# Kernel tuning notes

Hardware: AMD Instinct MI355X
Metric: run time of the kernel (lower is better)

Reference implementation:

```python
import jax, jax.numpy as jnp
import numpy as np

B, S, D, R, H, NI, NP, NO, K = 2, 2048, 1024, 1024, 8, 8, 32, 8, 3
DH = R // H


def setup_inputs() -> dict:
    key = jax.random.key(0)
    ks = jax.random.split(key, 32)
    rn = lambda k, shp, s=1.0: jax.random.normal(k, shp, jnp.float32) * s
    nrm = lambda v: v / (jnp.linalg.norm(v, axis=-1, keepdims=True) + 1e-8)
    w = 1.0 / np.sqrt(D).astype(np.float32)
    inp = {
        'x': rn(ks[0], (B, S, D)),
        'mask': jnp.tril(jnp.ones((S, S), bool))[None, None],  # causal [1,1,S,S]
        'Wr_in': rn(ks[1], (NI, D), w), 'Wr_proc': rn(ks[2], (NP, D), w), 'Wr_out': rn(ks[3], (NO, D), w),
        'WrO_in': rn(ks[4], (NI, R), w), 'WrO_proc': rn(ks[5], (NP, R), w), 'WrO_out': rn(ks[6], (NO, R), w),
        'Wq_in': rn(ks[7], (NI, D, R), w), 'vq': nrm(rn(ks[8], (NP, R))), 'Wq_out': rn(ks[9], (NO, R, D), w),
        'Wk_in': rn(ks[10], (NI, D, R), w), 'vk': nrm(rn(ks[11], (NP, R))), 'Wk_out': rn(ks[12], (NO, R, D), w),
        'Wv_in': rn(ks[13], (NI, D, R), w), 'vv': nrm(rn(ks[14], (NP, R))), 'Wv_out': rn(ks[15], (NO, R, D), w),
        # circuit_O = NeuronCircuit(rank, d_model): dims swapped
        'Wo_in': rn(ks[16], (NI, R, D), w), 'vo': nrm(rn(ks[17], (NP, D))), 'Wo_out': rn(ks[18], (NO, D, R), w),
    }
    return inp


def _router(x, Wi, Wp, Wo, k):
    in_w = jax.nn.softmax(x @ Wi.T, axis=-1)            # [B,S,NI]
    _, proc_idx = jax.lax.top_k(x @ Wp.T, k)            # [B,S,k]
    out_w = jax.nn.softmax(x @ Wo.T, axis=-1)           # [B,S,NO]
    return in_w, proc_idx, out_w


def _circuit(x, Win, vproc, Wout, in_w, proc_idx, out_w):
    # soft input mix: d_in -> r
    h = jnp.einsum('bsd,ndr,bsn->bsr', x, Win, in_w)
    # k sequential Householder reflections with gathered vectors
    v = vproc[proc_idx]                                 # [B,S,k,r]
    v = v / jnp.sqrt(jnp.sum(v * v, axis=-1, keepdims=True) + 1e-8)
    for i in range(v.shape[2]):
        vi = v[:, :, i, :]
        h = h - 2.0 * vi * jnp.sum(h * vi, axis=-1, keepdims=True)
    # soft output mix: r -> d_out
    return jnp.einsum('bsr,nrd,bsn->bsd', h, Wout, out_w)


def reference(x, mask, Wr_in, Wr_proc, Wr_out, WrO_in, WrO_proc, WrO_out,
              Wq_in, vq, Wq_out, Wk_in, vk, Wk_out, Wv_in, vv, Wv_out,
              Wo_in, vo, Wo_out):
    in_w, pidx, out_w = _router(x, Wr_in, Wr_proc, Wr_out, K)
    Q = _circuit(x, Wq_in, vq, Wq_out, in_w, pidx, out_w)   # [B,S,R]
    Kt = _circuit(x, Wk_in, vk, Wk_out, in_w, pidx, out_w)
    V = _circuit(x, Wv_in, vv, Wv_out, in_w, pidx, out_w)
    q = Q.reshape(B, S, H, DH).transpose(0, 2, 1, 3)
    k = Kt.reshape(B, S, H, DH).transpose(0, 2, 1, 3)
    v = V.reshape(B, S, H, DH).transpose(0, 2, 1, 3)
    scores = jnp.einsum('bhqd,bhkd->bhqk', q, k) / np.sqrt(DH).astype(np.float32)
    scores = jnp.where(mask, scores, jnp.float32(-1e9))
    p = jax.nn.softmax(scores, axis=-1)
    o = jnp.einsum('bhqk,bhkd->bhqd', p, v)
    o = o.transpose(0, 2, 1, 3).reshape(B, S, R)
    in_wO, pidxO, out_wO = _router(o, WrO_in, WrO_proc, WrO_out, K)
    out = _circuit(o, Wo_in, vo, Wo_out, in_wO, pidxO, out_wO)  # [B,S,D]
    return out
```

## Files before the change

### kernel.cpp

```cpp
#include <hip/hip_runtime.h>


typedef __attribute__((ext_vector_type(4))) float f32x4;
typedef _Float16 f16x8 __attribute__((ext_vector_type(8)));
typedef _Float16 f16x4 __attribute__((ext_vector_type(4)));

static constexpr int S_LEN  = 2048;
static constexpr int TOK    = 4096;
static constexpr int DMODEL = 1024;
static constexpr int KDIM   = 8192;

__device__ __forceinline__ void async16(const void* g, void* l) {
  __builtin_amdgcn_global_load_lds(
      (const __attribute__((address_space(1))) void*)g,
      (__attribute__((address_space(3))) void*)l, 16, 0, 0);
}

__global__ __launch_bounds__(256) void transpose_split(const float* __restrict__ W,
                                                       _Float16* __restrict__ Th,
                                                       _Float16* __restrict__ Tl) {
  __shared__ float tbuf[64][65];
  const int tid = threadIdx.x;
  const int k0 = blockIdx.x * 64, n0 = blockIdx.y * 64;
#pragma unroll
  for (int j = 0; j < 4; ++j) {
    int ci = tid + 256 * j;
    int r = ci >> 4, c4 = (ci & 15) * 4;
    float4 v = *(const float4*)&W[(size_t)(k0 + r) * DMODEL + n0 + c4];
    tbuf[r][c4 + 0] = v.x; tbuf[r][c4 + 1] = v.y;
    tbuf[r][c4 + 2] = v.z; tbuf[r][c4 + 3] = v.w;
  }
  __syncthreads();
#pragma unroll
  for (int j = 0; j < 2; ++j) {
    int ci = tid + 256 * j;
    int nl = ci >> 3, k8 = (ci & 7) * 8;
    f16x8 hv, lv;
#pragma unroll
    for (int e = 0; e < 8; ++e) {
      float v = tbuf[k8 + e][nl];
      _Float16 hh = (_Float16)v;
      hv[e] = hh;
      lv[e] = (_Float16)(v - (float)hh);
    }
    size_t off = (size_t)(n0 + nl) * KDIM + k0 + k8;
    *(f16x8*)&Th[off] = hv;
    if (Tl != nullptr) *(f16x8*)&Tl[off] = lv;
  }
}

__global__ __launch_bounds__(256) void router_kernel(const float* __restrict__ X,
                                                     const float* __restrict__ Wi,
                                                     const float* __restrict__ Wp,
                                                     const float* __restrict__ Wo,
                                                     float* __restrict__ in_w,
                                                     float* __restrict__ out_w,
                                                     int* __restrict__ pidx,
                                                     _Float16* __restrict__ Xh,
                                                     _Float16* __restrict__ Xl) {
  __shared__ float xs[1024];
  __shared__ double lg[48];
  const int t = blockIdx.x, tid = threadIdx.x;
  const int wid = tid >> 6, lane = tid & 63;
#pragma unroll
  for (int j = 0; j < 4; ++j) {
    int d = tid + 256 * j;
    xs[d] = X[(size_t)t * DMODEL + d];
  }
  __syncthreads();
  for (int i = wid; i < 48; i += 4) {
    const float* wrow = (i < 8)  ? Wi + (size_t)i * DMODEL
                      : (i < 40) ? Wp + (size_t)(i - 8) * DMODEL
                                 : Wo + (size_t)(i - 40) * DMODEL;
    double s = 0.0;
#pragma unroll
    for (int j = 0; j < 16; ++j) { int d = lane + 64 * j; s += (double)xs[d] * (double)wrow[d]; }
#pragma unroll
    for (int mm = 32; mm >= 1; mm >>= 1) s += __shfl_xor(s, mm);
    if (lane == 0) lg[i] = s;
  }
  __syncthreads();
  if (tid == 0) {
    float l[8], m;
    for (int i = 0; i < 8; ++i) l[i] = (float)lg[i];
    m = l[0];
    for (int i = 1; i < 8; ++i) m = fmaxf(m, l[i]);
    float e[8], su = 0.f;
    for (int i = 0; i < 8; ++i) { e[i] = expf(l[i] - m); su += e[i]; }
    for (int i = 0; i < 8; ++i) in_w[t * 8 + i] = e[i] / su;
  } else if (tid == 64) {
    float l[8], m;
    for (int i = 0; i < 8; ++i) l[i] = (float)lg[40 + i];
    m = l[0];
    for (int i = 1; i < 8; ++i) m = fmaxf(m, l[i]);
    float e[8], su = 0.f;
    for (int i = 0; i < 8; ++i) { e[i] = expf(l[i] - m); su += e[i]; }
    for (int i = 0; i < 8; ++i) out_w[t * 8 + i] = e[i] / su;
  } else if (tid == 128) {
    unsigned used = 0;
    for (int j = 0; j < 3; ++j) {
      double best = -1e300; int bi = 0;
      for (int i = 0; i < 32; ++i)
        if (!((used >> i) & 1u) && lg[8 + i] > best) { best = lg[8 + i]; bi = i; }
      used |= 1u << bi;
      pidx[t * 3 + j] = bi;
    }
  }
  if (Xh != nullptr) {
#pragma unroll
    for (int j = 0; j < 4; ++j) {
      int d = tid + 256 * j;
      float v = xs[d];
      _Float16 hh = (_Float16)v;
      Xh[(size_t)t * DMODEL + d] = hh;
      Xl[(size_t)t * DMODEL + d] = (_Float16)(v - (float)hh);
    }
  }
}

__global__ __launch_bounds__(256) void reflect4_kernel(const float* __restrict__ Pa,
                                                       const float* __restrict__ Pb,
                                                       const float* __restrict__ Pc,
                                                       const float* __restrict__ Pd,
                                                       const int* __restrict__ pidx,
                                                       const float* __restrict__ vtab,
                                                       _Float16* __restrict__ Hh,
                                                       _Float16* __restrict__ Hl) {
  __shared__ float red[8];
  const int t = blockIdx.x, tid = threadIdx.x;
  const int wid = tid >> 6, lane = tid & 63;
  size_t gi = (size_t)t * DMODEL + tid * 4;
  float4 ha = *(const float4*)&Pa[gi];
  float4 hb = *(const float4*)&Pb[gi];
  float4 hc = *(const float4*)&Pc[gi];
  float4 hd = *(const float4*)&Pd[gi];
  float4 h = {ha.x + hb.x + hc.x + hd.x, ha.y + hb.y + hc.y + hd.y,
              ha.z + hb.z + hc.z + hd.z, ha.w + hb.w + hc.w + hd.w};
  for (int i = 0; i < 3; ++i) {
    int idx = pidx[t * 3 + i];
    float4 vi = *(const float4*)&vtab[(size_t)idx * DMODEL + tid * 4];
    float hv = h.x * vi.x + h.y * vi.y + h.z * vi.z + h.w * vi.w;
    float vv = vi.x * vi.x + vi.y * vi.y + vi.z * vi.z + vi.w * vi.w;
#pragma unroll
    for (int mm = 32; mm >= 1; mm >>= 1) { hv += __shfl_xor(hv, mm); vv += __shfl_xor(vv, mm); }
    if (lane == 0) { red[wid] = hv; red[4 + wid] = vv; }
    __syncthreads();
    float dot = red[0] + red[1] + red[2] + red[3];
    float vn  = red[4] + red[5] + red[6] + red[7];
    __syncthreads();
    float c = 2.f * dot / (vn + 1e-8f);
    h.x -= c * vi.x; h.y -= c * vi.y; h.z -= c * vi.z; h.w -= c * vi.w;
  }
  float a[4] = {h.x, h.y, h.z, h.w};
  f16x4 hv4, lv4;
#pragma unroll
  for (int e = 0; e < 4; ++e) {
    _Float16 hh = (_Float16)a[e];
    hv4[e] = hh;
    lv4[e] = (_Float16)(a[e] - (float)hh);
  }
  *(f16x4*)&Hh[gi] = hv4;
  *(f16x4*)&Hl[gi] = lv4;
}

__global__ __launch_bounds__(256) void reduce4_planes(const float* __restrict__ a,
                                                      const float* __restrict__ b,
                                                      const float* __restrict__ c,
                                                      const float* __restrict__ d,
                                                      _Float16* __restrict__ Dh,
                                                      _Float16* __restrict__ Dl) {
  size_t i = ((size_t)blockIdx.x * 256 + threadIdx.x) * 4;
  float4 va = *(const float4*)&a[i];
  float4 vb = *(const float4*)&b[i];
  float4 vc = *(const float4*)&c[i];
  float4 vd = *(const float4*)&d[i];
  float s[4] = {va.x + vb.x + vc.x + vd.x, va.y + vb.y + vc.y + vd.y,
                va.z + vb.z + vc.z + vd.z, va.w + vb.w + vc.w + vd.w};
  f16x4 hv, lv;
#pragma unroll
  for (int e = 0; e < 4; ++e) {
    _Float16 hh = (_Float16)s[e];
    hv[e] = hh;
    lv[e] = (_Float16)(s[e] - (float)hh);
  }
  *(f16x4*)&Dh[i] = hv;
  *(f16x4*)&Dl[i] = lv;
}

__global__ __launch_bounds__(256) void reduce4_f32(const float* __restrict__ a,
                                                   const float* __restrict__ b,
                                                   const float* __restrict__ c,
                                                   const float* __restrict__ d,
                                                   float* __restrict__ o) {
  size_t i = ((size_t)blockIdx.x * 256 + threadIdx.x) * 4;
  float4 va = *(const float4*)&a[i];
  float4 vb = *(const float4*)&b[i];
  float4 vc = *(const float4*)&c[i];
  float4 vd = *(const float4*)&d[i];
  float4 vo = {va.x + vb.x + vc.x + vd.x, va.y + vb.y + vc.y + vd.y,
               va.z + vb.z + vc.z + vd.z, va.w + vb.w + vc.w + vd.w};
  *(float4*)&o[i] = vo;
}

template <bool FAST>
__global__ __launch_bounds__(512, 2) void gemm_planes(const _Float16* __restrict__ Ahp,
                                                      const _Float16* __restrict__ Alp,
                                                      const float* __restrict__ wmix,
                                                      const _Float16* __restrict__ Bh,
                                                      const _Float16* __restrict__ Bl,
                                                      float* __restrict__ C0,
                                                      float* __restrict__ C1,
                                                      float* __restrict__ C2,
                                                      float* __restrict__ C3) {
  __shared__ _Float16 sAh[2][256 * 32];
  __shared__ _Float16 sBh[2][256 * 32];
  __shared__ _Float16 sAl[2][FAST ? 8 : 256 * 32];
  __shared__ _Float16 sBl[2][FAST ? 8 : 256 * 32];
  __shared__ float sWr[256 * 2];
  const int tid = threadIdx.x;
  const int wid = tid >> 6, lane = tid & 63;
  const int l16 = lane & 15, lhi = lane >> 4;
  const int wr = wid >> 2, wc = wid & 3;
  const int fid = blockIdx.x + (blockIdx.y << 4) + (blockIdx.z << 6);
  const int wg  = ((fid & 7) << 5) + (fid >> 3);
  const int bm = (wg & 15) * 256;
  const int bn = ((wg >> 4) & 3) * 256;
  const int kz = wg >> 6;
  const int kbase = kz * 2048, nb = kz * 2;
  float* __restrict__ Cp = (kz == 0) ? C0 : (kz == 1) ? C1 : (kz == 2) ? C2 : C3;

  {
    int row = tid >> 1, p = tid & 1;
    const float* w = &wmix[(size_t)(bm + row) * 8 + nb];
    sWr[tid] = p ? w[1] : w[0] / w[1];
  }

  f32x4 acc[8][4];
#pragma unroll
  for (int i = 0; i < 8; ++i)
#pragma unroll
    for (int j = 0; j < 4; ++j) { f32x4 z = {0.f, 0.f, 0.f, 0.f}; acc[i][j] = z; }

  auto STAGE = [&](int buf, int kt) {
    const int kg = kbase + kt, d0 = kg & 1023;
#pragma unroll
    for (int j = 0; j < 2; ++j) {
      int ci = tid + 512 * j;
      int row = ci >> 2, jc = ci & 3;
      int jcs = jc ^ ((row >> 1) & 3);
      size_t ga = (size_t)(bm + row) * DMODEL + d0 + jcs * 8;
      size_t gb = (size_t)(bn + row) * KDIM + kg + jcs * 8;
      async16(&Ahp[ga], &sAh[buf][ci * 8]);
      async16(&Bh[gb],  &sBh[buf][ci * 8]);
      if constexpr (!FAST) {
        async16(&Alp[ga], &sAl[buf][ci * 8]);
        async16(&Bl[gb],  &sBl[buf][ci * 8]);
      }
    }
  };

  auto COMPUTE = [&](int buf) {
    __builtin_amdgcn_s_setprio(1);
    f16x8 b_h[4], b_l[4];
#pragma unroll
    for (int ni = 0; ni < 4; ++ni) {
      int row = wc * 64 + ni * 16 + l16;
      int idx = row * 32 + ((lhi ^ ((row >> 1) & 3)) * 8);
      b_h[ni] = *(const f16x8*)&sBh[buf][idx];
      if constexpr (!FAST) b_l[ni] = *(const f16x8*)&sBl[buf][idx];
    }
#pragma unroll
    for (int mi = 0; mi < 8; ++mi) {
      int rowa = wr * 128 + mi * 16 + l16;
      int idxa = rowa * 32 + ((lhi ^ ((rowa >> 1) & 3)) * 8);
      f16x8 a_h = *(const f16x8*)&sAh[buf][idxa];
      f16x8 a_l;
      if constexpr (!FAST) a_l = *(const f16x8*)&sAl[buf][idxa];
#pragma unroll
      for (int ni = 0; ni < 4; ++ni) {
        f32x4 a = acc[mi][ni];
        a = __builtin_amdgcn_mfma_f32_16x16x32_f16(a_h, b_h[ni], a, 0, 0, 0);
        if constexpr (!FAST) {
          a = __builtin_amdgcn_mfma_f32_16x16x32_f16(a_h, b_l[ni], a, 0, 0, 0);
          a = __builtin_amdgcn_mfma_f32_16x16x32_f16(a_l, b_h[ni], a, 0, 0, 0);
        }
        acc[mi][ni] = a;
      }
    }
    __builtin_amdgcn_s_setprio(0);
  };

  STAGE(0, 0);
  for (int t = 0; t < 63; ++t) {
    STAGE((t + 1) & 1, (t + 1) * 32);
    if constexpr (FAST) asm volatile("s_waitcnt vmcnt(4)" ::: "memory");
    else                asm volatile("s_waitcnt vmcnt(8)" ::: "memory");
    __builtin_amdgcn_s_barrier();
    __builtin_amdgcn_sched_barrier(0);
    COMPUTE(t & 1);
    if (t == 31) {
#pragma unroll
      for (int mi = 0; mi < 8; ++mi)
#pragma unroll
        for (int r = 0; r < 4; ++r) {
          float s = sWr[(wr * 128 + mi * 16 + lhi * 4 + r) * 2];
#pragma unroll
          for (int ni = 0; ni < 4; ++ni) acc[mi][ni][r] *= s;
        }
    }
    __builtin_amdgcn_s_barrier();
  }
  asm volatile("s_waitcnt vmcnt(0)" ::: "memory");
  __builtin_amdgcn_s_barrier();
  __builtin_amdgcn_sched_barrier(0);
  COMPUTE(1);

#pragma unroll
  for (int mi = 0; mi < 8; ++mi)
#pragma unroll
    for (int r = 0; r < 4; ++r) {
      int rowl = wr * 128 + mi * 16 + lhi * 4 + r;
      float s = sWr[rowl * 2 + 1];
#pragma unroll
      for (int ni = 0; ni < 4; ++ni) {
        int col = bn + wc * 64 + ni * 16 + l16;
        Cp[(size_t)(bm + rowl) * DMODEL + col] = acc[mi][ni][r] * s;
      }
    }
}

__global__ __launch_bounds__(256) void vtrans4_kernel(const float* __restrict__ Va,
                                                      const float* __restrict__ Vb,
                                                      const float* __restrict__ Vc,
                                                      const float* __restrict__ Vd,
                                                      _Float16* __restrict__ Vth,
                                                      _Float16* __restrict__ Vtl) {
  __shared__ float tbuf[64][65];
  const int tid = threadIdx.x;
  const int t0 = blockIdx.x * 64, d0 = blockIdx.y * 64, bh = blockIdx.z;
  const int b = bh >> 3, h = bh & 7;
#pragma unroll
  for (int j = 0; j < 4; ++j) {
    int ci = tid + 256 * j;
    int r = ci >> 4, c4 = (ci & 15) * 4;
    size_t g = (size_t)(b * S_LEN + t0 + r) * DMODEL + h * 128 + d0 + c4;
    float4 va = *(const float4*)&Va[g];
    float4 vb = *(const float4*)&Vb[g];
    float4 vc = *(const float4*)&Vc[g];
    float4 vd = *(const float4*)&Vd[g];
    tbuf[r][c4 + 0] = va.x + vb.x + vc.x + vd.x;
    tbuf[r][c4 + 1] = va.y + vb.y + vc.y + vd.y;
    tbuf[r][c4 + 2] = va.z + vb.z + vc.z + vd.z;
    tbuf[r][c4 + 3] = va.w + vb.w + vc.w + vd.w;
  }
  __syncthreads();
#pragma unroll
  for (int j = 0; j < 4; ++j) {
    int ci = tid + 256 * j;
    int r = ci >> 4, c4 = (ci & 15) * 4;
    float s[4] = {tbuf[c4 + 0][r], tbuf[c4 + 1][r], tbuf[c4 + 2][r], tbuf[c4 + 3][r]};
    f16x4 hv, lv;
#pragma unroll
    for (int e = 0; e < 4; ++e) {
      _Float16 hh = (_Float16)s[e];
      hv[e] = hh;
      lv[e] = (_Float16)(s[e] - (float)hh);
    }
    size_t o = ((size_t)bh * 128 + d0 + r) * S_LEN + t0 + c4;
    *(f16x4*)&Vth[o] = hv;
    *(f16x4*)&Vtl[o] = lv;
  }
}

__global__ __launch_bounds__(256) void attn_kernel(const _Float16* __restrict__ Qh,
                                                   const _Float16* __restrict__ Ql,
                                                   const _Float16* __restrict__ Kh,
                                                   const _Float16* __restrict__ Kl,
                                                   const _Float16* __restrict__ Vth,
                                                   const _Float16* __restrict__ Vtl,
                                                   float* __restrict__ O,
                                                   _Float16* __restrict__ Oh) {
  __shared__ _Float16 sKh[32 * 128], sKl[32 * 128];
  __shared__ _Float16 sVh[128 * 32], sVl[128 * 32];
  __shared__ _Float16 sPh[4 * 16 * 32], sPl[4 * 16 * 32];
  const int tid = threadIdx.x;
  const int wid = tid >> 6, lane = tid & 63;
  const int l16 = lane & 15, lhi = lane >> 4;
  const int qt = (gridDim.x - 1) - blockIdx.x;
  const int bh = blockIdx.y;
  const int b = bh >> 3, h = bh & 7;
  const size_t qkbase = (size_t)b * S_LEN * DMODEL + h * 128;
  const float scale = 0.08838834764831845f;

  const int qrow = qt * 64 + wid * 16 + l16;
  const size_t qoff = qkbase + (size_t)qrow * DMODEL;
  f16x8 qh[4], ql[4];
#pragma unroll
  for (int kk = 0; kk < 4; ++kk) {
    qh[kk] = *(const f16x8*)&Qh[qoff + kk * 32 + lhi * 8];
    ql[kk] = *(const f16x8*)&Ql[qoff + kk * 32 + lhi * 8];
  }

  f32x4 of[8];
#pragma unroll
  for (int i = 0; i < 8; ++i) { f32x4 z = {0.f, 0.f, 0.f, 0.f}; of[i] = z; }
  float m_[4], l_[4];
#pragma unroll
  for (int r = 0; r < 4; ++r) { m_[r] = -1e30f; l_[r] = 0.f; }

  const int ntw = qt * 2 + 1 + (wid >> 1);
  const int NT  = qt * 2 + 2;

  for (int kt = 0; kt < NT; ++kt) {
    __syncthreads();
#pragma unroll
    for (int j = 0; j < 2; ++j) {
      int ci = tid + 256 * j;
      int k = ci >> 4, c = ci & 15;
      int cs = c ^ (k & 7);
      size_t g = qkbase + (size_t)(kt * 32 + k) * DMODEL + cs * 8;
      async16(&Kh[g], &sKh[k * 128 + c * 8]);
      async16(&Kl[g], &sKl[k * 128 + c * 8]);
    }
#pragma unroll
    for (int j = 0; j < 2; ++j) {
      int ci = tid + 256 * j;
      int d = ci >> 2, c = ci & 3;
      int cs = c ^ ((d >> 1) & 3);
      size_t g = ((size_t)bh * 128 + d) * S_LEN + kt * 32 + cs * 8;
      async16(&Vth[g], &sVh[d * 32 + c * 8]);
      async16(&Vtl[g], &sVl[d * 32 + c * 8]);
    }
    __syncthreads();

    if (kt < ntw) {
      f32x4 s0 = {0.f, 0.f, 0.f, 0.f}, s1 = {0.f, 0.f, 0.f, 0.f};
#pragma unroll
      for (int kk = 0; kk < 4; ++kk) {
        int col = (kk * 32 + lhi * 8);
        int i0 = l16 * 128 + (col ^ ((l16 & 7) * 8));
        int i1 = (16 + l16) * 128 + (col ^ (((16 + l16) & 7) * 8));
        f16x8 kb0h = *(const f16x8*)&sKh[i0];
        f16x8 kb0l = *(const f16x8*)&sKl[i0];
        f16x8 kb1h = *(const f16x8*)&sKh[i1];
        f16x8 kb1l = *(const f16x8*)&sKl[i1];
        s0 = __builtin_amdgcn_mfma_f32_16x16x32_f16(qh[kk], kb0h, s0, 0, 0, 0);
        s0 = __builtin_amdgcn_mfma_f32_16x16x32_f16(qh[kk], kb0l, s0, 0, 0, 0);
        s0 = __builtin_amdgcn_mfma_f32_16x16x32_f16(ql[kk], kb0h, s0, 0, 0, 0);
        s1 = __builtin_amdgcn_mfma_f32_16x16x32_f16(qh[kk], kb1h, s1, 0, 0, 0);
        s1 = __builtin_amdgcn_mfma_f32_16x16x32_f16(qh[kk], kb1l, s1, 0, 0, 0);
        s1 = __builtin_amdgcn_mfma_f32_16x16x32_f16(ql[kk], kb1h, s1, 0, 0, 0);
      }
      const int qg = qt * 64 + wid * 16 + (lane >> 4) * 4;
      if (kt == ntw - 1) {
#pragma unroll
        for (int r = 0; r < 4; ++r) {
          int q = qg + r;
          int k0 = kt * 32 + l16, k1 = k0 + 16;
          s0[r] = (k0 <= q) ? s0[r] * scale : -1e30f;
          s1[r] = (k1 <= q) ? s1[r] * scale : -1e30f;
        }
      } else {
#pragma unroll
        for (int r = 0; r < 4; ++r) { s0[r] *= scale; s1[r] *= scale; }
      }
      float p0[4], p1[4], fr[4];
#pragma unroll
      for (int r = 0; r < 4; ++r) {
        float rm = fmaxf(s0[r], s1[r]);
        rm = fmaxf(rm, __shfl_xor(rm, 1));
        rm = fmaxf(rm, __shfl_xor(rm, 2));
        rm = fmaxf(rm, __shfl_xor(rm, 4));
        rm = fmaxf(rm, __shfl_xor(rm, 8));
        float mn = fmaxf(m_[r], rm);
        fr[r] = __expf(m_[r] - mn);
        m_[r] = mn;
        p0[r] = __expf(s0[r] - mn);
        p1[r] = __expf(s1[r] - mn);
        float rs = p0[r] + p1[r];
        rs += __shfl_xor(rs, 1);
        rs += __shfl_xor(rs, 2);
        rs += __shfl_xor(rs, 4);
        rs += __shfl_xor(rs, 8);
        l_[r] = l_[r] * fr[r] + rs;
      }
#pragma unroll
      for (int i = 0; i < 8; ++i)
#pragma unroll
        for (int r = 0; r < 4; ++r) of[i][r] *= fr[r];
#pragma unroll
      for (int r = 0; r < 4; ++r) {
        int q = (lane >> 4) * 4 + r;
        int swz = ((q >> 1) & 3) * 8;
        int c0 = l16, c1 = 16 + l16;
        _Float16 h0 = (_Float16)p0[r];
        _Float16 h1 = (_Float16)p1[r];
        sPh[wid * 512 + q * 32 + (c0 ^ swz)] = h0;
        sPl[wid * 512 + q * 32 + (c0 ^ swz)] = (_Float16)(p0[r] - (float)h0);
        sPh[wid * 512 + q * 32 + (c1 ^ swz)] = h1;
        sPl[wid * 512 + q * 32 + (c1 ^ swz)] = (_Float16)(p1[r] - (float)h1);
      }
      int pidxr = wid * 512 + l16 * 32 + ((lhi * 8) ^ (((l16 >> 1) & 3) * 8));
      f16x8 pah = *(const f16x8*)&sPh[pidxr];
      f16x8 pal = *(const f16x8*)&sPl[pidxr];
#pragma unroll
      for (int d16 = 0; d16 < 8; ++d16) {
        int d = d16 * 16 + l16;
        int vidx = d * 32 + ((lhi * 8) ^ (((d >> 1) & 3) * 8));
        f16x8 vbh = *(const f16x8*)&sVh[vidx];
        f16x8 vbl = *(const f16x8*)&sVl[vidx];
        f32x4 a = of[d16];
        a = __builtin_amdgcn_mfma_f32_16x16x32_f16(pah, vbh, a, 0, 0, 0);
        a = __builtin_amdgcn_mfma_f32_16x16x32_f16(pah, vbl, a, 0, 0, 0);
        a = __builtin_amdgcn_mfma_f32_16x16x32_f16(pal, vbh, a, 0, 0, 0);
        of[d16] = a;
      }
    }
  }
  float inv[4];
#pragma unroll
  for (int r = 0; r < 4; ++r) inv[r] = 1.f / l_[r];
  const int qg = qt * 64 + wid * 16 + (lane >> 4) * 4;
#pragma unroll
  for (int d16 = 0; d16 < 8; ++d16)
#pragma unroll
    for (int r = 0; r < 4; ++r) {
      float val = of[d16][r] * inv[r];
      size_t gi = qkbase + (size_t)(qg + r) * DMODEL + d16 * 16 + l16;
      O[gi] = val;
      Oh[gi] = (_Float16)val;
    }
}

extern "C" void kernel_launch(void* const* d_in, const int* in_sizes, int n_in,
                              void* d_out, int out_size, void* d_ws, size_t ws_size,
                              hipStream_t stream) {
  (void)in_sizes; (void)n_in; (void)out_size;
  const float* x        = (const float*)d_in[0];
  const float* Wr_in    = (const float*)d_in[2];
  const float* Wr_proc  = (const float*)d_in[3];
  const float* Wr_out   = (const float*)d_in[4];
  const float* WrO_in   = (const float*)d_in[5];
  const float* WrO_proc = (const float*)d_in[6];
  const float* WrO_out  = (const float*)d_in[7];
  const float* Wq_in    = (const float*)d_in[8];
  const float* vq       = (const float*)d_in[9];
  const float* Wq_out   = (const float*)d_in[10];
  const float* Wk_in    = (const float*)d_in[11];
  const float* vk       = (const float*)d_in[12];
  const float* Wk_out   = (const float*)d_in[13];
  const float* Wv_in    = (const float*)d_in[14];
  const float* vv       = (const float*)d_in[15];
  const float* Wv_out   = (const float*)d_in[16];
  const float* Wo_in    = (const float*)d_in[17];
  const float* vo       = (const float*)d_in[18];
  const float* Wo_out   = (const float*)d_in[19];

  char* wsbase = (char*)d_ws;
  size_t off = 0;
  auto carve = [&](size_t bytes) -> void* {
    void* r = wsbase + off;
    off = (off + bytes + 255) & ~(size_t)255;
    return r;
  };
  const size_t WBYTES = (size_t)KDIM * DMODEL * 2;
  const size_t PBYTES = (size_t)TOK * DMODEL * 2;
  const size_t HBYTES = (size_t)TOK * DMODEL * 4;
  _Float16* WTh = (_Float16*)carve(WBYTES);
  _Float16* WTl = (_Float16*)carve(WBYTES);
  _Float16* Xh  = (_Float16*)carve(PBYTES);
  _Float16* Xl  = (_Float16*)carve(PBYTES);
  _Float16* Hh  = (_Float16*)carve(PBYTES);
  _Float16* Hl  = (_Float16*)carve(PBYTES);
  float* P0 = (float*)carve(HBYTES);
  float* P1 = (float*)carve(HBYTES);
  float* P2 = (float*)carve(HBYTES);
  _Float16* Qph = (_Float16*)carve(PBYTES);
  _Float16* Qpl = (_Float16*)carve(PBYTES);
  _Float16* Kph = (_Float16*)carve(PBYTES);
  _Float16* Kpl = (_Float16*)carve(PBYTES);
  float* iw1 = (float*)carve((size_t)TOK * 8 * 4);
  float* ow1 = (float*)carve((size_t)TOK * 8 * 4);
  float* iw2 = (float*)carve((size_t)TOK * 8 * 4);
  float* ow2 = (float*)carve((size_t)TOK * 8 * 4);
  int* pi1 = (int*)carve((size_t)TOK * 3 * 4);
  int* pi2 = (int*)carve((size_t)TOK * 3 * 4);

  if (off > ws_size) {
    hipMemsetAsync(d_out, 0, (size_t)out_size * 4, stream);
    return;
  }

  float*    Pd  = (float*)d_out;
  float*    PQ  = (float*)Qph;
  float*    PX  = (float*)Xh;
  _Float16* Vth = WTh;
  _Float16* Vtl = WTh + (size_t)TOK * DMODEL;
  float*    Ofp = P0;
  _Float16* Ohp = (_Float16*)P1;

  const dim3 blk(256);
  const dim3 gblk(512);
  const dim3 tgrid(KDIM / 64, DMODEL / 64);
  const dim3 ggrid(TOK / 256, DMODEL / 256, 4);
  const dim3 rgrid(TOK * DMODEL / (256 * 4));
  const dim3 vgrid(S_LEN / 64, 2, 16);
  const dim3 agrid(S_LEN / 64, 16);

  router_kernel<<<TOK, blk, 0, stream>>>(x, Wr_in, Wr_proc, Wr_out, iw1, ow1, pi1, Xh, Xl);

  transpose_split<<<tgrid, blk, 0, stream>>>(Wq_in, WTh, WTl);
  gemm_planes<false><<<ggrid, gblk, 0, stream>>>(Xh, Xl, iw1, WTh, WTl, P0, P1, P2, Pd);
  reflect4_kernel<<<TOK, blk, 0, stream>>>(P0, P1, P2, Pd, pi1, vq, Hh, Hl);
  transpose_split<<<tgrid, blk, 0, stream>>>(Wq_out, WTh, WTl);
  gemm_planes<false><<<ggrid, gblk, 0, stream>>>(Hh, Hl, ow1, WTh, WTl, P0, P1, P2, Pd);
  reduce4_planes<<<rgrid, blk, 0, stream>>>(P0, P1, P2, Pd, Qph, Qpl);

  transpose_split<<<tgrid, blk, 0, stream>>>(Wk_in, WTh, WTl);
  gemm_planes<false><<<ggrid, gblk, 0, stream>>>(Xh, Xl, iw1, WTh, WTl, P0, P1, P2, Pd);
  reflect4_kernel<<<TOK, blk, 0, stream>>>(P0, P1, P2, Pd, pi1, vk, Hh, Hl);
  transpose_split<<<tgrid, blk, 0, stream>>>(Wk_out, WTh, WTl);
  gemm_planes<false><<<ggrid, gblk, 0, stream>>>(Hh, Hl, ow1, WTh, WTl, P0, P1, P2, Pd);
  reduce4_planes<<<rgrid, blk, 0, stream>>>(P0, P1, P2, Pd, Kph, Kpl);

  transpose_split<<<tgrid, blk, 0, stream>>>(Wv_in, WTh, WTl);
  gemm_planes<false><<<ggrid, gblk, 0, stream>>>(Xh, Xl, iw1, WTh, WTl, P0, P1, P2, Pd);
  reflect4_kernel<<<TOK, blk, 0, stream>>>(P0, P1, P2, Pd, pi1, vv, Hh, Hl);
  transpose_split<<<tgrid, blk, 0, stream>>>(Wv_out, WTh, WTl);
  gemm_planes<false><<<ggrid, gblk, 0, stream>>>(Hh, Hl, ow1, WTh, WTl, P0, P1, P2, Pd);
  vtrans4_kernel<<<vgrid, blk, 0, stream>>>(P0, P1, P2, Pd, Vth, Vtl);

  attn_kernel<<<agrid, blk, 0, stream>>>(Qph, Qpl, Kph, Kpl, Vth, Vtl, Ofp, Ohp);

  router_kernel<<<TOK, blk, 0, stream>>>(Ofp, WrO_in, WrO_proc, WrO_out, iw2, ow2, pi2,
                                         nullptr, nullptr);
  transpose_split<<<tgrid, blk, 0, stream>>>(Wo_in, WTh, nullptr);
  gemm_planes<true><<<ggrid, gblk, 0, stream>>>(Ohp, Ohp, iw2, WTh, WTh, PX, P0, P2, Pd);
  reflect4_kernel<<<TOK, blk, 0, stream>>>(PX, P0, P2, Pd, pi2, vo, Hh, Hl);
  transpose_split<<<tgrid, blk, 0, stream>>>(Wo_out, WTh, nullptr);
  gemm_planes<true><<<ggrid, gblk, 0, stream>>>(Hh, Hh, ow2, WTh, WTh, P0, P1, P2, PQ);
  reduce4_f32<<<rgrid, blk, 0, stream>>>(P0, P1, P2, PQ, (float*)d_out);
}
```

Measured before the change: 1.645 ms.

## Split split-fp16 GEMM K-loop into two half-phases with staggered async loads

Restructures the GEMM main loop so that loads run two stages ahead instead of one. In the non-FAST path, each iteration is split into two phases: the Ah/Bh/Bl products run first, then the Al×Bh product, with the Al tile for stage t+2 issued only after the second phase. The aim is to overlap global-to-LDS transfers with MFMA work more finely and to shorten the wait at each barrier. The cost is extra barriers and more delicate vmcnt bookkeeping, which could stall or be wrong if a count is off.

```diff
diff --git a/kernel.cpp b/kernel.cpp
--- a/kernel.cpp
+++ b/kernel.cpp
@@ -241,7 +241,7 @@
 #pragma unroll
     for (int j = 0; j < 4; ++j) { f32x4 z = {0.f, 0.f, 0.f, 0.f}; acc[i][j] = z; }
 
-  auto STAGE = [&](int buf, int kt) {
+  auto STAGE_H0 = [&](int buf, int kt) {
     const int kg = kbase + kt, d0 = kg & 1023;
 #pragma unroll
     for (int j = 0; j < 2; ++j) {
@@ -252,68 +252,114 @@
       size_t gb = (size_t)(bn + row) * KDIM + kg + jcs * 8;
       async16(&Ahp[ga], &sAh[buf][ci * 8]);
       async16(&Bh[gb],  &sBh[buf][ci * 8]);
-      if constexpr (!FAST) {
-        async16(&Alp[ga], &sAl[buf][ci * 8]);
-        async16(&Bl[gb],  &sBl[buf][ci * 8]);
-      }
+      if constexpr (!FAST) async16(&Bl[gb], &sBl[buf][ci * 8]);
     }
   };
-
-  auto COMPUTE = [&](int buf) {
-    __builtin_amdgcn_s_setprio(1);
-    f16x8 b_h[4], b_l[4];
-#pragma unroll
-    for (int ni = 0; ni < 4; ++ni) {
-      int row = wc * 64 + ni * 16 + l16;
-      int idx = row * 32 + ((lhi ^ ((row >> 1) & 3)) * 8);
-      b_h[ni] = *(const f16x8*)&sBh[buf][idx];
-      if constexpr (!FAST) b_l[ni] = *(const f16x8*)&sBl[buf][idx];
-    }
-#pragma unroll
-    for (int mi = 0; mi < 8; ++mi) {
-      int rowa = wr * 128 + mi * 16 + l16;
-      int idxa = rowa * 32 + ((lhi ^ ((rowa >> 1) & 3)) * 8);
-      f16x8 a_h = *(const f16x8*)&sAh[buf][idxa];
-      f16x8 a_l;
-      if constexpr (!FAST) a_l = *(const f16x8*)&sAl[buf][idxa];
+  auto STAGE_H1 = [&](int buf, int kt) {
+    const int kg = kbase + kt, d0 = kg & 1023;
+#pragma unroll
+    for (int j = 0; j < 2; ++j) {
+      int ci = tid + 512 * j;
+      int row = ci >> 2, jc = ci & 3;
+      int jcs = jc ^ ((row >> 1) & 3);
+      size_t ga = (size_t)(bm + row) * DMODEL + d0 + jcs * 8;
+      async16(&Alp[ga], &sAl[buf][ci * 8]);
+    }
+  };
+
+  auto RESCALE = [&]() {
+#pragma unroll
+    for (int mi = 0; mi < 8; ++mi)
+#pragma unroll
+      for (int r = 0; r < 4; ++r) {
+        float s = sWr[(wr * 128 + mi * 16 + lhi * 4 + r) * 2];
+#pragma unroll
+        for (int ni = 0; ni < 4; ++ni) acc[mi][ni][r] *= s;
+      }
+  };
+
+  STAGE_H0(0, 0);
+  if constexpr (!FAST) STAGE_H1(0, 0);
+  STAGE_H0(1, 32);
+  if constexpr (!FAST) STAGE_H1(1, 32);
+
+  for (int t = 0; t < 64; ++t) {
+    const int buf = t & 1;
+    if constexpr (FAST) {
+      if (t < 63) asm volatile("s_waitcnt vmcnt(4)" ::: "memory");
+      else        asm volatile("s_waitcnt vmcnt(0)" ::: "memory");
+      __builtin_amdgcn_s_barrier();
+      __builtin_amdgcn_sched_barrier(0);
+      __builtin_amdgcn_s_setprio(1);
+      f16x8 b_h[4];
 #pragma unroll
       for (int ni = 0; ni < 4; ++ni) {
-        f32x4 a = acc[mi][ni];
-        a = __builtin_amdgcn_mfma_f32_16x16x32_f16(a_h, b_h[ni], a, 0, 0, 0);
-        if constexpr (!FAST) {
+        int row = wc * 64 + ni * 16 + l16;
+        b_h[ni] = *(const f16x8*)&sBh[buf][row * 32 + ((lhi ^ ((row >> 1) & 3)) * 8)];
+      }
+#pragma unroll
+      for (int mi = 0; mi < 8; ++mi) {
+        int rowa = wr * 128 + mi * 16 + l16;
+        f16x8 a_h = *(const f16x8*)&sAh[buf][rowa * 32 + ((lhi ^ ((rowa >> 1) & 3)) * 8)];
+#pragma unroll
+        for (int ni = 0; ni < 4; ++ni)
+          acc[mi][ni] = __builtin_amdgcn_mfma_f32_16x16x32_f16(a_h, b_h[ni], acc[mi][ni], 0, 0, 0);
+      }
+      __builtin_amdgcn_s_setprio(0);
+      if (t == 31) RESCALE();
+      __builtin_amdgcn_s_barrier();
+      if (t < 62) STAGE_H0(buf, (t + 2) * 32);
+    } else {
+      if (t < 63) asm volatile("s_waitcnt vmcnt(10)" ::: "memory");
+      else        asm volatile("s_waitcnt vmcnt(2)"  ::: "memory");
+      __builtin_amdgcn_s_barrier();
+      __builtin_amdgcn_sched_barrier(0);
+      __builtin_amdgcn_s_setprio(1);
+      f16x8 b_h[4], b_l[4];
+#pragma unroll
+      for (int ni = 0; ni < 4; ++ni) {
+        int row = wc * 64 + ni * 16 + l16;
+        int idx = row * 32 + ((lhi ^ ((row >> 1) & 3)) * 8);
+        b_h[ni] = *(const f16x8*)&sBh[buf][idx];
+        b_l[ni] = *(const f16x8*)&sBl[buf][idx];
+      }
+#pragma unroll
+      for (int mi = 0; mi < 8; ++mi) {
+        int rowa = wr * 128 + mi * 16 + l16;
+        f16x8 a_h = *(const f16x8*)&sAh[buf][rowa * 32 + ((lhi ^ ((rowa >> 1) & 3)) * 8)];
+#pragma unroll
+        for (int ni = 0; ni < 4; ++ni) {
+          f32x4 a = acc[mi][ni];
+          a = __builtin_amdgcn_mfma_f32_16x16x32_f16(a_h, b_h[ni], a, 0, 0, 0);
           a = __builtin_amdgcn_mfma_f32_16x16x32_f16(a_h, b_l[ni], a, 0, 0, 0);
-          a = __builtin_amdgcn_mfma_f32_16x16x32_f16(a_l, b_h[ni], a, 0, 0, 0);
+          acc[mi][ni] = a;
         }
-        acc[mi][ni] = a;
-      }
-    }
-    __builtin_amdgcn_s_setprio(0);
-  };
-
-  STAGE(0, 0);
-  for (int t = 0; t < 63; ++t) {
-    STAGE((t + 1) & 1, (t + 1) * 32);
-    if constexpr (FAST) asm volatile("s_waitcnt vmcnt(4)" ::: "memory");
-    else                asm volatile("s_waitcnt vmcnt(8)" ::: "memory");
-    __builtin_amdgcn_s_barrier();
-    __builtin_amdgcn_sched_barrier(0);
-    COMPUTE(t & 1);
-    if (t == 31) {
-#pragma unroll
-      for (int mi = 0; mi < 8; ++mi)
-#pragma unroll
-        for (int r = 0; r < 4; ++r) {
-          float s = sWr[(wr * 128 + mi * 16 + lhi * 4 + r) * 2];
-#pragma unroll
-          for (int ni = 0; ni < 4; ++ni) acc[mi][ni][r] *= s;
-        }
-    }
-    __builtin_amdgcn_s_barrier();
-  }
-  asm volatile("s_waitcnt vmcnt(0)" ::: "memory");
-  __builtin_amdgcn_s_barrier();
-  __builtin_amdgcn_sched_barrier(0);
-  COMPUTE(1);
+      }
+      __builtin_amdgcn_s_setprio(0);
+      __builtin_amdgcn_s_barrier();
+      __builtin_amdgcn_sched_barrier(0);
+      if (t < 62) STAGE_H0(buf, (t + 2) * 32);
+      if (t < 62)      asm volatile("s_waitcnt vmcnt(14)" ::: "memory");
+      else if (t == 62) asm volatile("s_waitcnt vmcnt(8)" ::: "memory");
+      else             asm volatile("s_waitcnt vmcnt(0)" ::: "memory");
+      __builtin_amdgcn_s_barrier();
+      __builtin_amdgcn_sched_barrier(0);
+      __builtin_amdgcn_s_setprio(1);
+#pragma unroll
+      for (int mi = 0; mi < 8; ++mi) {
+        int rowa = wr * 128 + mi * 16 + l16;
+        f16x8 a_l = *(const f16x8*)&sAl[buf][rowa * 32 + ((lhi ^ ((rowa >> 1) & 3)) * 8)];
+#pragma unroll
+        for (int ni = 0; ni < 4; ++ni)
+          acc[mi][ni] = __builtin_amdgcn_mfma_f32_16x16x32_f16(a_l, b_h[ni], acc[mi][ni], 0, 0, 0);
+      }
+      __builtin_amdgcn_s_setprio(0);
+      if (t == 31) RESCALE();
+      __builtin_amdgcn_s_barrier();
+      __builtin_amdgcn_sched_barrier(0);
+      if (t < 62) STAGE_H1(buf, (t + 2) * 32);
+    }
+  }
 
 #pragma unroll
   for (int mi = 0; mi < 8; ++mi)
```

New measurement: 1.744 ms. 6.0% more time.
